# Kernel tuning notes

Hardware: AMD Instinct MI355X
Metric: run time of the kernel (lower is better)

## Reference

```python
import jax, jax.numpy as jnp
import numpy as np

X_DIM, T_DIM = 64, 32

def setup_inputs() -> dict:
    key = jax.random.key(0)
    ks = jax.random.split(key, 9)
    B, N, H = 4, 512, 128
    s = lambda fan_in: 1.0 / np.sqrt(fan_in)
    return {
        "x": jax.random.normal(ks[0], (B, N, X_DIM), jnp.float32),
        "y": jax.random.normal(ks[1], (B, N, X_DIM), jnp.float32),
        "t": jax.random.normal(ks[2], (B, T_DIM), jnp.float32),
        "W1": jax.random.normal(ks[3], (X_DIM + T_DIM, H), jnp.float32) * s(X_DIM + T_DIM),
        "b1": jax.random.normal(ks[4], (H,), jnp.float32) * s(X_DIM + T_DIM),
        "W2": jax.random.normal(ks[5], (H, H), jnp.float32) * s(H),
        "b2": jax.random.normal(ks[6], (H,), jnp.float32) * s(H),
        "W3": jax.random.normal(ks[7], (H, 1), jnp.float32) * s(H),
        "b3": jax.random.normal(ks[8], (1,), jnp.float32) * s(H),
    }

def reference(x, y, t, W1, b1, W2, b2, W3, b3):
    # diff: [B, N, N, x_dim] pairwise squared differences (abs then square == square)
    diff = jnp.square(jnp.abs(x[:, :, None, :] - y[:, None, :, :]))
    # First linear layer applied without materializing the concat:
    # concat(diff, t_broadcast) @ W1 == diff @ W1[:X_DIM] + t @ W1[X_DIM:]
    h = jnp.einsum('bijd,dh->bijh', diff, W1[:X_DIM])
    h = h + jnp.einsum('bd,dh->bh', t, W1[X_DIM:])[:, None, None, :] + b1
    h = jax.nn.relu(h)
    h = jax.nn.relu(jnp.einsum('bijh,hk->bijk', h, W2) + b2)
    K = (jnp.einsum('bijh,hk->bijk', h, W3) + b3)[..., 0]  # [B, N, N]
    return K
```

## Files before the change

### kernel.cpp

```cpp
#include <hip/hip_runtime.h>

typedef _Float16 f16;
typedef _Float16 f16x2 __attribute__((ext_vector_type(2)));
typedef _Float16 f16x4 __attribute__((ext_vector_type(4)));
typedef _Float16 f16x8 __attribute__((ext_vector_type(8)));
typedef float f32x2 __attribute__((ext_vector_type(2)));
typedef float f32x4 __attribute__((ext_vector_type(4)));

#define MFMA16(A, B, C) __builtin_amdgcn_mfma_f32_16x16x32_f16((A), (B), (C), 0, 0, 0)

static __device__ __forceinline__ f16x2 cvt2(f32x2 v) {
    return __builtin_bit_cast(f16x2, __builtin_amdgcn_cvt_pkrtz(v.x, v.y));
}
static __device__ __forceinline__ f32x2 relu2(f32x2 v) {
    return __builtin_elementwise_max(v, f32x2{0.f, 0.f});
}
static __device__ __forceinline__ f16x8 pack8(f16x2 a, f16x2 b, f16x2 c, f16x2 d) {
    f16x4 lo = __builtin_shufflevector(a, b, 0, 1, 2, 3);
    f16x4 hi = __builtin_shufflevector(c, d, 0, 1, 2, 3);
    return __builtin_shufflevector(lo, hi, 0, 1, 2, 3, 4, 5, 6, 7);
}


__global__ __launch_bounds__(256, 1)
void pairmlp_kernel(const float* __restrict__ x, const float* __restrict__ y,
                    const float* __restrict__ t, const float* __restrict__ W1,
                    const float* __restrict__ b1, const float* __restrict__ W2,
                    const float* __restrict__ b2, const float* __restrict__ W3,
                    const float* __restrict__ b3, float* __restrict__ out)
{
    const int N = 512, H = 128, XD = 64, TD = 32;

    __shared__ f16x8 W1a[1024];
    __shared__ f16x8 W2a[2048];
    __shared__ f16x8 xt[256];
    __shared__ f16x8 yt[256];
    __shared__ float tbs[128];

    const int tid = threadIdx.x;
    const int b = blockIdx.z;
    const int ibase = blockIdx.y * 32;
    const int jbase = blockIdx.x * 32;

    for (int o = tid; o < 1024; o += 256) {
        int c = o & 15, g = (o >> 4) & 3, kh = o >> 6;
        int ks = kh & 1, ht = kh >> 1;
        int h = ht * 16 + c;
        f16x8 v;
#pragma unroll
        for (int i = 0; i < 8; ++i) {
            int d = 32 * ks + 8 * g + i;
            v[i] = (f16)W1[d * H + h];
        }
        W1a[o] = v;
    }
    for (int o = tid; o < 2048; o += 256) {
        int c = o & 15, g = (o >> 4) & 3, kh = o >> 6;
        int ks = kh & 3, hpt = kh >> 2;
        int hp = hpt * 16 + c;
        f16x8 v;
#pragma unroll
        for (int i = 0; i < 8; ++i) {
            int h = 32 * ks + ((i >> 2) << 4) + 4 * g + (i & 3);
            v[i] = (f16)W2[h * H + hp];
        }
        W2a[o] = v;
    }
    if (tid < 128) {
        float s = b1[tid];
#pragma unroll 8
        for (int d = 0; d < TD; ++d)
            s += t[b * TD + d] * W1[(XD + d) * H + tid];
        tbs[tid] = s;
    }
    {
        int o = tid;
        int r = o >> 3, q = o & 7;
        const float* xp = x + ((size_t)(b * N + ibase + r)) * XD + q * 8;
        f16x8 v;
#pragma unroll
        for (int e = 0; e < 8; ++e) v[e] = (f16)xp[e];
        xt[o] = v;
        const float* yp = y + ((size_t)(b * N + jbase + r)) * XD + q * 8;
        f16x8 u;
#pragma unroll
        for (int e = 0; e < 8; ++e) u[e] = (f16)yp[e];
        yt[r * 8 + (q ^ (r & 7))] = u;
    }
    __syncthreads();

    const int w = tid >> 6;
    const int l = tid & 63;
    const int c = l & 15;
    const int g = l >> 4;
    const float b3v = b3[0];

    f32x2 tbo2[4][4];
#pragma unroll
    for (int ks = 0; ks < 4; ++ks)
#pragma unroll
        for (int q = 0; q < 4; ++q) {
            int h0 = 32 * ks + 16 * (q >> 1) + 4 * g + 2 * (q & 1);
            tbo2[ks][q] = f32x2{tbs[h0], tbs[h0 + 1]};
        }
    f32x2 b2p[8][2];
    f16x2 w3p[8][2];
#pragma unroll
    for (int ht = 0; ht < 8; ++ht)
#pragma unroll
        for (int p = 0; p < 2; ++p) {
            int h0 = 16 * ht + 4 * g + 2 * p;
            b2p[ht][p] = f32x2{b2[h0], b2[h0 + 1]};
            w3p[ht][p] = f16x2{(f16)W3[h0], (f16)W3[h0 + 1]};
        }

    const f32x4 zc = f32x4{0.f, 0.f, 0.f, 0.f};

#pragma unroll 1
    for (int ci = 0; ci < 8; ++ci) {
        const int il = w * 8 + ci;

        f16x8 xv0 = xt[il * 8 + g];
        f16x8 xv1 = xt[il * 8 + 4 + g];

        f32x4 acc1[8][2];
#pragma unroll
        for (int ks = 0; ks < 2; ++ks) {
            f16x8 df[2];
#pragma unroll
            for (int mt = 0; mt < 2; ++mt) {
                int jl = 16 * mt + c;
                f16x8 yv = yt[jl * 8 + ((4 * ks + g) ^ (c & 7))];
                f16x8 dd = (ks ? xv1 : xv0) - yv;
                df[mt] = dd * dd;
            }
#pragma unroll
            for (int ht = 0; ht < 8; ++ht) {
                f16x8 a = W1a[(ht * 2 + ks) * 64 + g * 16 + c];
                if (ks == 0) {
                    acc1[ht][0] = MFMA16(a, df[0], zc);
                    acc1[ht][1] = MFMA16(a, df[1], zc);
                } else {
                    acc1[ht][0] = MFMA16(a, df[0], acc1[ht][0]);
                    acc1[ht][1] = MFMA16(a, df[1], acc1[ht][1]);
                }
            }
        }

        f16x8 bf2[4][2];
#pragma unroll
        for (int ks = 0; ks < 4; ++ks) {
#pragma unroll
            for (int mt = 0; mt < 2; ++mt) {
                f32x4 A = acc1[2 * ks][mt];
                f32x4 Bv = acc1[2 * ks + 1][mt];
                f32x2 r0 = relu2(f32x2{A[0], A[1]} + tbo2[ks][0]);
                f32x2 r1 = relu2(f32x2{A[2], A[3]} + tbo2[ks][1]);
                f32x2 r2 = relu2(f32x2{Bv[0], Bv[1]} + tbo2[ks][2]);
                f32x2 r3 = relu2(f32x2{Bv[2], Bv[3]} + tbo2[ks][3]);
                bf2[ks][mt] = pack8(cvt2(r0), cvt2(r1), cvt2(r2), cvt2(r3));
            }
        }

        f32x4 acc2[8][2];
#pragma unroll
        for (int ks = 0; ks < 4; ++ks) {
#pragma unroll
            for (int ht = 0; ht < 8; ++ht) {
                f16x8 a = W2a[(ht * 4 + ks) * 64 + g * 16 + c];
                if (ks == 0) {
                    acc2[ht][0] = MFMA16(a, bf2[0][0], zc);
                    acc2[ht][1] = MFMA16(a, bf2[0][1], zc);
                } else {
                    acc2[ht][0] = MFMA16(a, bf2[ks][0], acc2[ht][0]);
                    acc2[ht][1] = MFMA16(a, bf2[ks][1], acc2[ht][1]);
                }
            }
        }

        float s0 = 0.f, s1 = 0.f;
#pragma unroll
        for (int ht = 0; ht < 8; ++ht) {
            f32x4 A0 = acc2[ht][0];
            f32x4 A1 = acc2[ht][1];
#pragma unroll
            for (int p = 0; p < 2; ++p) {
                f32x2 e0 = relu2(f32x2{A0[2 * p], A0[2 * p + 1]} + b2p[ht][p]);
                f32x2 e1 = relu2(f32x2{A1[2 * p], A1[2 * p + 1]} + b2p[ht][p]);
                s0 = __builtin_amdgcn_fdot2(cvt2(e0), w3p[ht][p], s0, false);
                s1 = __builtin_amdgcn_fdot2(cvt2(e1), w3p[ht][p], s1, false);
            }
        }
        s0 += __shfl_xor(s0, 16);
        s0 += __shfl_xor(s0, 32);
        s1 += __shfl_xor(s1, 16);
        s1 += __shfl_xor(s1, 32);

        if (g == 0) {
            size_t base = ((size_t)(b * N + ibase + il)) * N + jbase;
            out[base + c]      = s0 + b3v;
            out[base + 16 + c] = s1 + b3v;
        }
    }
}

extern "C" void kernel_launch(void* const* d_in, const int* in_sizes, int n_in,
                              void* d_out, int out_size, void* d_ws, size_t ws_size,
                              hipStream_t stream) {
    const float* x  = (const float*)d_in[0];
    const float* y  = (const float*)d_in[1];
    const float* t  = (const float*)d_in[2];
    const float* W1 = (const float*)d_in[3];
    const float* b1 = (const float*)d_in[4];
    const float* W2 = (const float*)d_in[5];
    const float* b2 = (const float*)d_in[6];
    const float* W3 = (const float*)d_in[7];
    const float* b3 = (const float*)d_in[8];
    float* out = (float*)d_out;

    dim3 grid(16, 16, 4);
    dim3 block(256);
    pairmlp_kernel<<<grid, block, 0, stream>>>(x, y, t, W1, b1, W2, b2, W3, b3, out);
}
```

Before: 77.73 us.

## Widen j-tile to 64 and move bias/ReLU epilogues to packed fp16

Each block now covers 64 j columns instead of 32, which halves the grid and amortizes the per-block staging of W1/W2 into LDS over twice the work. Each wave reuses every weight fragment across four column tiles, and the second GEMM is split into two halves to limit accumulator register pressure. The bias-add and ReLU epilogues now run in packed fp16 after conversion instead of in fp32, which cuts VALU work but changes rounding slightly. The risks are higher register use and fewer blocks (512) to fill the GPU.

New measurement: 63.39 us. 1.23x faster.

```diff
diff --git a/kernel.cpp b/kernel.cpp
--- a/kernel.cpp
+++ b/kernel.cpp
@@ -12,12 +12,13 @@
 static __device__ __forceinline__ f16x2 cvt2(f32x2 v) {
     return __builtin_bit_cast(f16x2, __builtin_amdgcn_cvt_pkrtz(v.x, v.y));
 }
-static __device__ __forceinline__ f32x2 relu2(f32x2 v) {
-    return __builtin_elementwise_max(v, f32x2{0.f, 0.f});
-}
-static __device__ __forceinline__ f16x8 pack8(f16x2 a, f16x2 b, f16x2 c, f16x2 d) {
-    f16x4 lo = __builtin_shufflevector(a, b, 0, 1, 2, 3);
-    f16x4 hi = __builtin_shufflevector(c, d, 0, 1, 2, 3);
+static __device__ __forceinline__ f16x4 cvt4(f32x4 v) {
+    f16x2 a = cvt2(f32x2{v[0], v[1]});
+    f16x2 b = cvt2(f32x2{v[2], v[3]});
+    return __builtin_shufflevector(a, b, 0, 1, 2, 3);
+}
+static __device__ __forceinline__ f16x8 cvt8(f32x4 a, f32x4 b) {
+    f16x4 lo = cvt4(a), hi = cvt4(b);
     return __builtin_shufflevector(lo, hi, 0, 1, 2, 3, 4, 5, 6, 7);
 }
 
@@ -34,13 +35,13 @@
     __shared__ f16x8 W1a[1024];
     __shared__ f16x8 W2a[2048];
     __shared__ f16x8 xt[256];
-    __shared__ f16x8 yt[256];
+    __shared__ f16x8 yt[512];
     __shared__ float tbs[128];
 
     const int tid = threadIdx.x;
     const int b = blockIdx.z;
     const int ibase = blockIdx.y * 32;
-    const int jbase = blockIdx.x * 32;
+    const int jbase = blockIdx.x * 64;
 
     for (int o = tid; o < 1024; o += 256) {
         int c = o & 15, g = (o >> 4) & 3, kh = o >> 6;
@@ -81,6 +82,11 @@
 #pragma unroll
         for (int e = 0; e < 8; ++e) v[e] = (f16)xp[e];
         xt[o] = v;
+    }
+#pragma unroll
+    for (int oo = 0; oo < 2; ++oo) {
+        int o = tid + oo * 256;
+        int r = o >> 3, q = o & 7;
         const float* yp = y + ((size_t)(b * N + jbase + r)) * XD + q * 8;
         f16x8 u;
 #pragma unroll
@@ -95,26 +101,34 @@
     const int g = l >> 4;
     const float b3v = b3[0];
 
-    f32x2 tbo2[4][4];
-#pragma unroll
-    for (int ks = 0; ks < 4; ++ks)
-#pragma unroll
-        for (int q = 0; q < 4; ++q) {
-            int h0 = 32 * ks + 16 * (q >> 1) + 4 * g + 2 * (q & 1);
-            tbo2[ks][q] = f32x2{tbs[h0], tbs[h0 + 1]};
-        }
-    f32x2 b2p[8][2];
-    f16x2 w3p[8][2];
-#pragma unroll
-    for (int ht = 0; ht < 8; ++ht)
-#pragma unroll
-        for (int p = 0; p < 2; ++p) {
-            int h0 = 16 * ht + 4 * g + 2 * p;
-            b2p[ht][p] = f32x2{b2[h0], b2[h0 + 1]};
-            w3p[ht][p] = f16x2{(f16)W3[h0], (f16)W3[h0 + 1]};
-        }
+    f16x8 tbo[4];
+#pragma unroll
+    for (int ks = 0; ks < 4; ++ks) {
+        f16x8 v;
+#pragma unroll
+        for (int i = 0; i < 8; ++i) {
+            int h = 32 * ks + ((i >> 2) << 4) + 4 * g + (i & 3);
+            v[i] = (f16)tbs[h];
+        }
+        tbo[ks] = v;
+    }
+    f16x4 b2h[8], w3h[8];
+#pragma unroll
+    for (int ht = 0; ht < 8; ++ht) {
+        f16x4 bv, wv;
+#pragma unroll
+        for (int r = 0; r < 4; ++r) {
+            int h0 = 16 * ht + 4 * g + r;
+            bv[r] = (f16)b2[h0];
+            wv[r] = (f16)W3[h0];
+        }
+        b2h[ht] = bv;
+        w3h[ht] = wv;
+    }
 
     const f32x4 zc = f32x4{0.f, 0.f, 0.f, 0.f};
+    const f16x8 z8 = f16x8{};
+    const f16x4 z4 = f16x4{};
 
 #pragma unroll 1
     for (int ci = 0; ci < 8; ++ci) {
@@ -123,12 +137,12 @@
         f16x8 xv0 = xt[il * 8 + g];
         f16x8 xv1 = xt[il * 8 + 4 + g];
 
-        f32x4 acc1[8][2];
+        f32x4 acc1[8][4];
 #pragma unroll
         for (int ks = 0; ks < 2; ++ks) {
-            f16x8 df[2];
-#pragma unroll
-            for (int mt = 0; mt < 2; ++mt) {
+            f16x8 df[4];
+#pragma unroll
+            for (int mt = 0; mt < 4; ++mt) {
                 int jl = 16 * mt + c;
                 f16x8 yv = yt[jl * 8 + ((4 * ks + g) ^ (c & 7))];
                 f16x8 dd = (ks ? xv1 : xv0) - yv;
@@ -137,69 +151,68 @@
 #pragma unroll
             for (int ht = 0; ht < 8; ++ht) {
                 f16x8 a = W1a[(ht * 2 + ks) * 64 + g * 16 + c];
-                if (ks == 0) {
-                    acc1[ht][0] = MFMA16(a, df[0], zc);
-                    acc1[ht][1] = MFMA16(a, df[1], zc);
-                } else {
-                    acc1[ht][0] = MFMA16(a, df[0], acc1[ht][0]);
-                    acc1[ht][1] = MFMA16(a, df[1], acc1[ht][1]);
+#pragma unroll
+                for (int mt = 0; mt < 4; ++mt) {
+                    if (ks == 0) acc1[ht][mt] = MFMA16(a, df[mt], zc);
+                    else         acc1[ht][mt] = MFMA16(a, df[mt], acc1[ht][mt]);
                 }
             }
         }
 
-        f16x8 bf2[4][2];
-#pragma unroll
-        for (int ks = 0; ks < 4; ++ks) {
-#pragma unroll
-            for (int mt = 0; mt < 2; ++mt) {
-                f32x4 A = acc1[2 * ks][mt];
-                f32x4 Bv = acc1[2 * ks + 1][mt];
-                f32x2 r0 = relu2(f32x2{A[0], A[1]} + tbo2[ks][0]);
-                f32x2 r1 = relu2(f32x2{A[2], A[3]} + tbo2[ks][1]);
-                f32x2 r2 = relu2(f32x2{Bv[0], Bv[1]} + tbo2[ks][2]);
-                f32x2 r3 = relu2(f32x2{Bv[2], Bv[3]} + tbo2[ks][3]);
-                bf2[ks][mt] = pack8(cvt2(r0), cvt2(r1), cvt2(r2), cvt2(r3));
-            }
-        }
-
-        f32x4 acc2[8][2];
-#pragma unroll
-        for (int ks = 0; ks < 4; ++ks) {
-#pragma unroll
-            for (int ht = 0; ht < 8; ++ht) {
-                f16x8 a = W2a[(ht * 4 + ks) * 64 + g * 16 + c];
-                if (ks == 0) {
-                    acc2[ht][0] = MFMA16(a, bf2[0][0], zc);
-                    acc2[ht][1] = MFMA16(a, bf2[0][1], zc);
-                } else {
-                    acc2[ht][0] = MFMA16(a, bf2[ks][0], acc2[ht][0]);
-                    acc2[ht][1] = MFMA16(a, bf2[ks][1], acc2[ht][1]);
+        f16x8 bf2[4][4];
+#pragma unroll
+        for (int ks = 0; ks < 4; ++ks)
+#pragma unroll
+            for (int mt = 0; mt < 4; ++mt) {
+                f16x8 v = cvt8(acc1[2 * ks][mt], acc1[2 * ks + 1][mt]) + tbo[ks];
+                bf2[ks][mt] = __builtin_elementwise_max(v, z8);
+            }
+
+        float s0 = 0.f, s1 = 0.f, s2 = 0.f, s3 = 0.f;
+#pragma unroll
+        for (int half = 0; half < 2; ++half) {
+            f32x4 acc2[4][4];
+#pragma unroll
+            for (int ks = 0; ks < 4; ++ks) {
+#pragma unroll
+                for (int hh = 0; hh < 4; ++hh) {
+                    int ht = half * 4 + hh;
+                    f16x8 a = W2a[(ht * 4 + ks) * 64 + g * 16 + c];
+#pragma unroll
+                    for (int mt = 0; mt < 4; ++mt) {
+                        if (ks == 0) acc2[hh][mt] = MFMA16(a, bf2[0][mt], zc);
+                        else         acc2[hh][mt] = MFMA16(a, bf2[ks][mt], acc2[hh][mt]);
+                    }
                 }
             }
-        }
-
-        float s0 = 0.f, s1 = 0.f;
-#pragma unroll
-        for (int ht = 0; ht < 8; ++ht) {
-            f32x4 A0 = acc2[ht][0];
-            f32x4 A1 = acc2[ht][1];
-#pragma unroll
-            for (int p = 0; p < 2; ++p) {
-                f32x2 e0 = relu2(f32x2{A0[2 * p], A0[2 * p + 1]} + b2p[ht][p]);
-                f32x2 e1 = relu2(f32x2{A1[2 * p], A1[2 * p + 1]} + b2p[ht][p]);
-                s0 = __builtin_amdgcn_fdot2(cvt2(e0), w3p[ht][p], s0, false);
-                s1 = __builtin_amdgcn_fdot2(cvt2(e1), w3p[ht][p], s1, false);
-            }
-        }
-        s0 += __shfl_xor(s0, 16);
-        s0 += __shfl_xor(s0, 32);
-        s1 += __shfl_xor(s1, 16);
-        s1 += __shfl_xor(s1, 32);
+#pragma unroll
+            for (int hh = 0; hh < 4; ++hh) {
+                int ht = half * 4 + hh;
+                f16x2 wlo = __builtin_shufflevector(w3h[ht], w3h[ht], 0, 1);
+                f16x2 whi = __builtin_shufflevector(w3h[ht], w3h[ht], 2, 3);
+#pragma unroll
+                for (int mt = 0; mt < 4; ++mt) {
+                    f16x4 e = __builtin_elementwise_max(cvt4(acc2[hh][mt]) + b2h[ht], z4);
+                    f16x2 elo = __builtin_shufflevector(e, e, 0, 1);
+                    f16x2 ehi = __builtin_shufflevector(e, e, 2, 3);
+                    float* sp = (mt == 0) ? &s0 : (mt == 1) ? &s1 : (mt == 2) ? &s2 : &s3;
+                    *sp = __builtin_amdgcn_fdot2(elo, wlo, *sp, false);
+                    *sp = __builtin_amdgcn_fdot2(ehi, whi, *sp, false);
+                }
+            }
+        }
+
+        s0 += __shfl_xor(s0, 16); s0 += __shfl_xor(s0, 32);
+        s1 += __shfl_xor(s1, 16); s1 += __shfl_xor(s1, 32);
+        s2 += __shfl_xor(s2, 16); s2 += __shfl_xor(s2, 32);
+        s3 += __shfl_xor(s3, 16); s3 += __shfl_xor(s3, 32);
 
         if (g == 0) {
             size_t base = ((size_t)(b * N + ibase + il)) * N + jbase;
             out[base + c]      = s0 + b3v;
             out[base + 16 + c] = s1 + b3v;
+            out[base + 32 + c] = s2 + b3v;
+            out[base + 48 + c] = s3 + b3v;
         }
     }
 }
@@ -218,7 +231,7 @@
     const float* b3 = (const float*)d_in[8];
     float* out = (float*)d_out;
 
-    dim3 grid(16, 16, 4);
+    dim3 grid(8, 16, 4);
     dim3 block(256);
     pairmlp_kernel<<<grid, block, 0, stream>>>(x, y, t, W1, b1, W2, b2, W3, b3, out);
 }
```
